# Kernel tuning notes

Measured on AMD Instinct MI355X. Metric: run time of the kernel, lower is better.

## Reference

```python
import jax, jax.numpy as jnp
import numpy as np

B, T, D = 2, 4096, 1024
H, HD = 16, 64
KV = H * HD  # 1024


def setup_inputs() -> dict:
    key = jax.random.key(0)
    ks = jax.random.split(key, 6)
    sc = lambda k, shape, s: jax.random.normal(k, shape, jnp.float32) * s
    return {
        "x": sc(ks[0], (B, T, D), 1.0),
        "W_in": sc(ks[1], (D, 4 * KV), D ** -0.5),      # in_proj (in, out) layout
        "W_ba": sc(ks[2], (D, 2 * H), D ** -0.5),       # ba_proj
        "conv_w": sc(ks[3], (3 * KV, 1, 4), 0.5),       # depthwise conv, (O, I/groups=1, K)
        "dt_bias": jnp.ones((H,), jnp.float32),
        "A_log": jnp.log(jax.random.uniform(ks[4], (H,), jnp.float32, 1e-3, 16.0)),
        "norm_w": jnp.ones((HD,), jnp.float32),
        "W_o": sc(ks[5], (KV, D), KV ** -0.5),
    }


def _l2norm(t, eps=1e-6):
    return t * jax.lax.rsqrt(jnp.sum(t * t, axis=-1, keepdims=True) + eps)


def reference(x, W_in, W_ba, conv_w, dt_bias, A_log, norm_w, W_o):
    Bb, Tt, _ = x.shape
    qkvz = x @ W_in                                  # [B,T,4*KV]
    q, k, v, z = jnp.split(qkvz, 4, axis=-1)
    b, a = jnp.split(x @ W_ba, 2, axis=-1)           # [B,T,H] each

    # causal depthwise conv (kernel 4, left pad 3) + SiLU on concat(q,k,v)
    qkv = jnp.concatenate([q, k, v], axis=-1).transpose(0, 2, 1)  # [B,3KV,T]
    qkv = jax.lax.conv_general_dilated(
        qkv, conv_w, window_strides=(1,), padding=[(3, 0)],
        feature_group_count=3 * KV, dimension_numbers=("NCH", "OIH", "NCH"))
    qkv = jax.nn.silu(qkv).transpose(0, 2, 1)        # [B,T,3KV]
    q, k, v = jnp.split(qkv, 3, axis=-1)

    rs = lambda t: t.reshape(Bb, Tt, H, HD)
    q, k, v, z = rs(q), rs(k), rs(v), rs(z)

    beta = jax.nn.sigmoid(b)                         # [B,T,H]
    A = jnp.exp(jnp.maximum(A_log, -2.3))            # [H]
    g = -A * jax.nn.softplus(a + dt_bias)            # [B,T,H], log decay <= 0

    # fla use_qk_l2norm_in_kernel=True: l2-normalize q,k; q scaled by d^-0.5
    q = _l2norm(q) * (HD ** -0.5)
    k = _l2norm(k)

    # gated delta rule recurrence over time (state S: [B,H,dk,dv])
    tm = lambda t: jnp.swapaxes(t, 0, 1)             # time-major

    def step(S, inp):
        qt, kt, vt, gt, bt = inp
        S = S * jnp.exp(gt)[..., None, None]
        pred = jnp.einsum("bhk,bhkv->bhv", kt, S)
        S = S + jnp.einsum("bhk,bhv->bhkv", kt, (vt - pred) * bt[..., None])
        o = jnp.einsum("bhk,bhkv->bhv", qt, S)
        return S, o

    S0 = jnp.zeros((Bb, H, HD, HD), jnp.float32)
    _, y = jax.lax.scan(step, S0, (tm(q), tm(k), tm(v), tm(g), tm(beta)))
    y = jnp.swapaxes(y, 0, 1)                        # [B,T,H,HD]

    # RMSNormGated over head_dim, gated by silu(z)
    y = y * jax.lax.rsqrt(jnp.mean(y * y, axis=-1, keepdims=True) + 1e-6)
    y = (norm_w * y) * jax.nn.silu(z)

    return y.reshape(Bb, Tt, KV) @ W_o
```

## Files before the change

kernel.cpp:

```cpp
#include <hip/hip_runtime.h>

typedef unsigned short u16;
typedef unsigned int u32;
typedef __attribute__((ext_vector_type(8))) __bf16 bf16x8;
typedef __attribute__((ext_vector_type(8))) _Float16 f16x8;
typedef __attribute__((ext_vector_type(4))) _Float16 f16x4;
typedef __attribute__((ext_vector_type(4))) float f32x4;

#define DEV __device__ __forceinline__

DEV u16 f2bf(float f) {
  u32 u = __float_as_uint(f);
  u += 0x7FFFu + ((u >> 16) & 1u);
  return (u16)(u >> 16);
}
DEV float bf2f(u16 h) { return __uint_as_float(((u32)h) << 16); }
DEV void splitbf(float f, u16& hi, u16& lo) {
  u16 h = f2bf(f);
  hi = h;
  lo = f2bf(f - bf2f(h));
}
DEV void split4(float4 v, ushort4& hh, ushort4& ll) {
  splitbf(v.x, hh.x, ll.x);
  splitbf(v.y, hh.y, ll.y);
// ... 334 lines not shown
  __syncthreads();
#pragma unroll
  for (int i = 0; i < 4; ++i)
#pragma unroll
    for (int j = 0; j < 4; ++j)
#pragma unroll
      for (int r = 0; r < 4; ++r) {
        int t = i * 16 + rbase + r, s = j * 16 + lrow;
        Af[t * 64 + s] = (s < t) ? bs[t] * expf(gcs[t] - gcs[s]) * acc[i][j][r] : 0.f;
      }
  __syncthreads();
  float x[64];
#pragma unroll
  for (int t = 0; t < 64; ++t) {
    float sum = 0.f;
#pragma unroll
    for (int s4 = 0; s4 + 4 <= t; s4 += 4) {
      float4 a4 = *(const float4*)&Af[t * 64 + s4];
      sum += a4.x * x[s4] + a4.y * x[s4 + 1] + a4.z * x[s4 + 2] + a4.w * x[s4 + 3];
    }
#pragma unroll
    for (int s = (t & ~3); s < t; ++s) sum += Af[t * 64 + s] * x[s];
    x[t] = ((t == lane) ? 1.f : 0.f) - sum;
  }
#pragma unroll
  for (int t = 0; t < 64; ++t) {
    u16 hi, lo;
    splitbf(x[t], hi, lo);
    Tgh[(size_t)bhc * 4096 + SW(t, lane)] = hi;
    Tgl[(size_t)bhc * 4096 + SW(t, lane)] = lo;
  }
}

__global__ __launch_bounds__(256) void k_mn(const u16* __restrict__ khG, const u16* __restrict__ klG,
                                            const u16* __restrict__ vhG, const u16* __restrict__ vlG,
                                            const u16* __restrict__ Tgh, const u16* __restrict__ Tgl,
                                            const float* __restrict__ gcG, const float* __restrict__ betaG,
                                            u16* __restrict__ Mh, u16* __restrict__ Ml,
                                            u16* __restrict__ Nh, u16* __restrict__ Nl) {
  extern __shared__ __align__(16) char smem[];
  u16* base = (u16*)smem;
  u16* Tbh  = base + 0 * 4096;
  u16* Tbl  = base + 1 * 4096;
  u16* X1h  = base + 2 * 4096;
  u16* X1l  = base + 3 * 4096;
  u16* KdTh = base + 4 * 4096;
  u16* KdTl = base + 5 * 4096;
  u16* X2h  = base + 6 * 4096;
  u16* X2l  = base + 7 * 4096;
  float* gcs = (float*)(base + 8 * 4096);
  float* bs  = gcs + 64;

  const int bhc = blockIdx.x;
  const int c = bhc & 63, h = (bhc >> 6) & 15, bb = bhc >> 10;
  const int tid = threadIdx.x, w = tid >> 6, l = tid & 63;
  const int lrow = l & 15, lk8 = (l >> 4) * 8, rbase = (l >> 4) * 4;
  const int t0 = c * 64;
  const size_t rowbase = (size_t)bb * 4096;
  const size_t ktile = (size_t)bhc * 4096;

  if (tid < 64) {
    gcs[tid] = gcG[(size_t)bhc * 64 + tid];
    bs[tid] = betaG[(rowbase + t0 + tid) * 16 + h];
  }
#pragma unroll
  for (int i = 0; i < 2; ++i) {
    const int idx = tid + 256 * i;
    const int off = idx * 8;
    *(float4*)&Tbh[off] = *(const float4*)&Tgh[(size_t)bhc * 4096 + off];
    *(float4*)&Tbl[off] = *(const float4*)&Tgl[(size_t)bhc * 4096 + off];
  }
  __syncthreads();
  const float gc63 = gcs[63];
#pragma unroll
  for (int i = 0; i < 16; ++i) {
    const int flat = tid + 256 * i;
    const int s = flat >> 6, d = flat & 63;
    const int sws = SW(s, d);
    const float kf = bf2f(khG[ktile + sws]) + bf2f(klG[ktile + sws]);
    const float gv = gcs[s], bv = bs[s];
    u16 hh, ll;
    splitbf(bv * expf(gv) * kf, hh, ll);
    X1h[SW(d, s)] = hh; X1l[SW(d, s)] = ll;
    splitbf(expf(gc63 - gv) * kf, hh, ll);
    KdTh[SW(d, s)] = hh; KdTl[SW(d, s)] = ll;
    const float vv = bf2f(vhG[ktile + sws]) + bf2f(vlG[ktile + sws]);
    splitbf(bv * vv, hh, ll);
    X2h[SW(d, s)] = hh; X2l[SW(d, s)] = ll;
  }
  __syncthreads();

  f32x4 aW[4], aU[4];
#pragma unroll
  for (int j = 0; j < 4; ++j) { aW[j] = {0.f,0.f,0.f,0.f}; aU[j] = {0.f,0.f,0.f,0.f}; }
#pragma unroll
  for (int ks = 0; ks < 2; ++ks) {
    const int ao = SW(w * 16 + lrow, ks * 32 + lk8);
    bf16x8 aTh = *(const bf16x8*)&Tbh[ao];
    bf16x8 aTl = *(const bf16x8*)&Tbl[ao];
#pragma unroll
    for (int j = 0; j < 4; ++j) {
      const int bo = SW(j * 16 + lrow, ks * 32 + lk8);
      aW[j] = mm3(aTh, aTl, *(const bf16x8*)&X1h[bo], *(const bf16x8*)&X1l[bo], aW[j]);
      aU[j] = mm3(aTh, aTl, *(const bf16x8*)&X2h[bo], *(const bf16x8*)&X2l[bo], aU[j]);
    }
  }
  __syncthreads();
#pragma unroll
  for (int j = 0; j < 4; ++j)
#pragma unroll
    for (int r = 0; r < 4; ++r) {
      const int t = w * 16 + rbase + r, dcol = j * 16 + lrow;
      u16 hh, ll;
      splitbf(aW[j][r], hh, ll);
      X1h[SW(dcol, t)] = hh; X1l[SW(dcol, t)] = ll;
      splitbf(aU[j][r], hh, ll);
      X2h[SW(dcol, t)] = hh; X2l[SW(dcol, t)] = ll;
    }
  __syncthreads();

  f32x4 aM[4], aN[4];
#pragma unroll
  for (int j = 0; j < 4; ++j) { aM[j] = {0.f,0.f,0.f,0.f}; aN[j] = {0.f,0.f,0.f,0.f}; }
#pragma unroll
  for (int ks = 0; ks < 2; ++ks) {
    const int ao = SW(w * 16 + lrow, ks * 32 + lk8);
    bf16x8 aKh = *(const bf16x8*)&KdTh[ao];
    bf16x8 aKl = *(const bf16x8*)&KdTl[ao];
#pragma unroll
    for (int j = 0; j < 4; ++j) {
      const int bo = SW(j * 16 + lrow, ks * 32 + lk8);
      aM[j] = mm3(aKh, aKl, *(const bf16x8*)&X1h[bo], *(const bf16x8*)&X1l[bo], aM[j]);
      aN[j] = mm3(aKh, aKl, *(const bf16x8*)&X2h[bo], *(const bf16x8*)&X2l[bo], aN[j]);
    }
  }
  __syncthreads();
  const float decC = expf(gc63);
#pragma unroll
  for (int j = 0; j < 4; ++j)
#pragma unroll
    for (int r = 0; r < 4; ++r) {
      const int d = w * 16 + rbase + r, d2 = j * 16 + lrow;
      u16 hh, ll;
      splitbf(((d == d2) ? decC : 0.f) - aM[j][r], hh, ll);
      X1h[SW(d, d2)] = hh; X1l[SW(d, d2)] = ll;
      splitbf(aN[j][r], hh, ll);
      X2h[SW(d, d2)] = hh; X2l[SW(d, d2)] = ll;
    }
  __syncthreads();
#pragma unroll
  for (int i = 0; i < 2; ++i) {
    const int idx = tid + 256 * i;
    const int off = idx * 8;
    *(float4*)&Mh[(size_t)bhc * 4096 + off] = *(const float4*)&X1h[off];
    *(float4*)&Ml[(size_t)bhc * 4096 + off] = *(const float4*)&X1l[off];
    *(float4*)&Nh[(size_t)bhc * 4096 + off] = *(const float4*)&X2h[off];
    *(float4*)&Nl[(size_t)bhc * 4096 + off] = *(const float4*)&X2l[off];
  }
}

__global__ __launch_bounds__(256) void k_seg(const u16* __restrict__ Mh, const u16* __restrict__ Ml,
                                             const u16* __restrict__ Nh, const u16* __restrict__ Nl,
                                             u16* __restrict__ Msegh, u16* __restrict__ Msegl,
                                             u16* __restrict__ Nsegh, u16* __restrict__ Nsegl) {
  extern __shared__ __align__(16) char smem[];
  u16* base = (u16*)smem;
  u16* MaTh = base + 0 * 4096;
  u16* MaTl = base + 1 * 4096;
  u16* NaTh = base + 2 * 4096;
  u16* NaTl = base + 3 * 4096;
  u16* sMh  = base + 4 * 4096;
  u16* sMl  = base + 5 * 4096;
  u16* sNh  = base + 6 * 4096;
  u16* sNl  = base + 7 * 4096;

  const int blk = blockIdx.x;
  const size_t cbase = (size_t)(blk >> 3) * 64 + (blk & 7) * 8;
  const int tid = threadIdx.x, w = tid >> 6, l = tid & 63;
  const int lrow = l & 15, lk8 = (l >> 4) * 8, rbase = (l >> 4) * 4;

#pragma unroll
  for (int i = 0; i < 2; ++i) {
    const int off = (tid + 256 * i) * 8;
    *(float4*)&sMh[off] = *(const float4*)&Mh[cbase * 4096 + off];
    *(float4*)&sMl[off] = *(const float4*)&Ml[cbase * 4096 + off];
    *(float4*)&sNh[off] = *(const float4*)&Nh[cbase * 4096 + off];
    *(float4*)&sNl[off] = *(const float4*)&Nl[cbase * 4096 + off];
  }
  __syncthreads();
#pragma unroll
  for (int i = 0; i < 16; ++i) {
    const int flat = tid + 256 * i;
    const int a = flat >> 6, b = flat & 63;
    MaTh[SW(a, b)] = sMh[SW(b, a)];
    MaTl[SW(a, b)] = sMl[SW(b, a)];
    NaTh[SW(a, b)] = sNh[SW(b, a)];
    NaTl[SW(a, b)] = sNl[SW(b, a)];
  }
  __syncthreads();

  for (int j = 1; j < 8; ++j) {
#pragma unroll
    for (int i = 0; i < 2; ++i) {
      const int off = (tid + 256 * i) * 8;
      *(float4*)&sMh[off] = *(const float4*)&Mh[(cbase + j) * 4096 + off];
      *(float4*)&sMl[off] = *(const float4*)&Ml[(cbase + j) * 4096 + off];
      *(float4*)&sNh[off] = *(const float4*)&Nh[(cbase + j) * 4096 + off];
      *(float4*)&sNl[off] = *(const float4*)&Nl[(cbase + j) * 4096 + off];
    }
    __syncthreads();
    f32x4 aM2[4], aN2[4];
#pragma unroll
    for (int jj = 0; jj < 4; ++jj) { aM2[jj] = {0.f,0.f,0.f,0.f}; aN2[jj] = {0.f,0.f,0.f,0.f}; }
#pragma unroll
    for (int ks = 0; ks < 2; ++ks) {
      const int ao = SW(w * 16 + lrow, ks * 32 + lk8);
      bf16x8 aCh = *(const bf16x8*)&sMh[ao];
      bf16x8 aCl = *(const bf16x8*)&sMl[ao];
#pragma unroll
      for (int jj = 0; jj < 4; ++jj) {
        const int bo = SW(jj * 16 + lrow, ks * 32 + lk8);
        aM2[jj] = mm3(aCh, aCl, *(const bf16x8*)&MaTh[bo], *(const bf16x8*)&MaTl[bo], aM2[jj]);
        aN2[jj] = mm3(aCh, aCl, *(const bf16x8*)&NaTh[bo], *(const bf16x8*)&NaTl[bo], aN2[jj]);
      }
    }
    __syncthreads();
#pragma unroll
    for (int jj = 0; jj < 4; ++jj)
#pragma unroll
      for (int r = 0; r < 4; ++r) {
        const int t = w * 16 + rbase + r, col = jj * 16 + lrow;
        u16 hh, ll;
        splitbf(aM2[jj][r], hh, ll);
        MaTh[SW(col, t)] = hh; MaTl[SW(col, t)] = ll;
        const float nv = aN2[jj][r] + bf2f(sNh[SW(t, col)]) + bf2f(sNl[SW(t, col)]);
        splitbf(nv, hh, ll);
        NaTh[SW(col, t)] = hh; NaTl[SW(col, t)] = ll;
      }
    __syncthreads();
  }
#pragma unroll
  for (int i = 0; i < 16; ++i) {
    const int flat = tid + 256 * i;
    const int t = flat >> 6, s = flat & 63;
    Msegh[(size_t)blk * 4096 + SW(t, s)] = MaTh[SW(s, t)];
    Msegl[(size_t)blk * 4096 + SW(t, s)] = MaTl[SW(s, t)];
    Nsegh[(size_t)blk * 4096 + SW(t, s)] = NaTh[SW(s, t)];
    Nsegl[(size_t)blk * 4096 + SW(t, s)] = NaTl[SW(s, t)];
  }
}

__global__ __launch_bounds__(256) void k_bound(const u16* __restrict__ Msegh, const u16* __restrict__ Msegl,
                                               const u16* __restrict__ Nsegh, const u16* __restrict__ Nsegl,
                                               u16* __restrict__ Ssegh, u16* __restrict__ Ssegl) {
  __shared__ __align__(16) u16 STh[4096], STl[4096];
  __shared__ __align__(16) u16 sMh[4096], sMl[4096], sNh[4096], sNl[4096];
  const int bh = blockIdx.x;
  const int tid = threadIdx.x, w = tid >> 6, l = tid & 63;
  const int lrow = l & 15, lk8 = (l >> 4) * 8, rbase = (l >> 4) * 4;
  for (int i = tid; i < 4096; i += 256) { STh[i] = (u16)0; STl[i] = (u16)0; }
  __syncthreads();
  for (int j = 0; j < 8; ++j) {
    const size_t sb = (size_t)(bh * 8 + j) * 4096;
#pragma unroll
    for (int i = 0; i < 2; ++i) {
      const int off = (tid + 256 * i) * 8;
      *(float4*)&Ssegh[sb + off] = *(const float4*)&STh[off];
      *(float4*)&Ssegl[sb + off] = *(const float4*)&STl[off];
      *(float4*)&sMh[off] = *(const float4*)&Msegh[sb + off];
      *(float4*)&sMl[off] = *(const float4*)&Msegl[sb + off];
      *(float4*)&sNh[off] = *(const float4*)&Nsegh[sb + off];
      *(float4*)&sNl[off] = *(const float4*)&Nsegl[sb + off];
    }
    __syncthreads();
    f32x4 acc[4];
#pragma unroll
    for (int jj = 0; jj < 4; ++jj) acc[jj] = {0.f, 0.f, 0.f, 0.f};
#pragma unroll
    for (int ks = 0; ks < 2; ++ks) {
      const int ao = SW(w * 16 + lrow, ks * 32 + lk8);
      bf16x8 aSh = *(const bf16x8*)&STh[ao];
      bf16x8 aSl = *(const bf16x8*)&STl[ao];
#pragma unroll
      for (int jj = 0; jj < 4; ++jj) {
        const int bo = SW(jj * 16 + lrow, ks * 32 + lk8);
        acc[jj] = mm3(aSh, aSl, *(const bf16x8*)&sMh[bo], *(const bf16x8*)&sMl[bo], acc[jj]);
      }
    }
    __syncthreads();
#pragma unroll
    for (int jj = 0; jj < 4; ++jj)
#pragma unroll
      for (int r = 0; r < 4; ++r) {
        const int v = w * 16 + rbase + r, t = jj * 16 + lrow;
        const float sv = acc[jj][r] + bf2f(sNh[SW(t, v)]) + bf2f(sNl[SW(t, v)]);
        u16 hh, ll;
        splitbf(sv, hh, ll);
        STh[SW(v, t)] = hh; STl[SW(v, t)] = ll;
      }
    __syncthreads();
  }
}

__global__ __launch_bounds__(256, 1) void k_scan2(const u16* __restrict__ qhG, const u16* __restrict__ qlG,
                                               const u16* __restrict__ khG, const u16* __restrict__ klG,
                                               const u16* __restrict__ vhG, const u16* __restrict__ vlG,
                                               const u16* __restrict__ zb,
                                               const u16* __restrict__ Tgh, const u16* __restrict__ Tgl,
                                               const float* __restrict__ gcG,
                                               const float* __restrict__ betaG, const float* __restrict__ norm_w,
                                               const u16* __restrict__ Ssegh, const u16* __restrict__ Ssegl,
                                               u16* __restrict__ Yhi, u16* __restrict__ Ylo) {
  extern __shared__ __align__(16) char smem[];
  u16* base = (u16*)smem;
  u16* Kbh  = base + 0 * 4096;
  u16* Kbl  = base + 1 * 4096;
  u16* Qbh  = base + 2 * 4096;
  u16* Qbl  = base + 3 * 4096;
  u16* Vbh  = base + 4 * 4096;
  u16* Vbl  = base + 5 * 4096;
  u16* Zb   = base + 6 * 4096;
  u16* Tbh  = base + 7 * 4096;
  u16* Tbl  = base + 8 * 4096;
  u16* SbTh = base + 9 * 4096;
  u16* SbTl = base + 10 * 4096;
  u16* Mqh  = base + 11 * 4096;
  u16* Mql  = base + 12 * 4096;
  u16* KdTh = base + 13 * 4096;
  u16* KdTl = base + 14 * 4096;
  u16* RTh  = base + 15 * 4096;
  u16* RTl  = base + 16 * 4096;
  u16* UTh  = base + 17 * 4096;
  u16* UTl  = base + 18 * 4096;
  u16* Ybh  = RTh;
  u16* Ybl  = RTl;
  float* gcs = (float*)(base + 19 * 4096);
  float* bs  = gcs + 64;
  float* nws = gcs + 128;

  const int blk = blockIdx.x;
  const int bh = blk >> 3, seg = blk & 7;
  const int bb = bh >> 4, h = bh & 15;
  const int tid = threadIdx.x, w = tid >> 6, l = tid & 63;
  const int lrow = l & 15, lk8 = (l >> 4) * 8, rbase = (l >> 4) * 4;
  const size_t rowbase = (size_t)bb * 4096;
  const size_t bhTile = (size_t)bh * 64;

  {
    const int c = seg * 8, t0 = c * 64;
    const size_t gt = (bhTile + c) * 4096;
#pragma unroll
    for (int i = 0; i < 2; ++i) {
      const int o8 = (tid + 256 * i) * 8;
      GLDS16(qhG + gt + o8, &Qbh[o8]);
      GLDS16(qlG + gt + o8, &Qbl[o8]);
      GLDS16(khG + gt + o8, &Kbh[o8]);
      GLDS16(klG + gt + o8, &Kbl[o8]);
      GLDS16(vhG + gt + o8, &Vbh[o8]);
      GLDS16(vlG + gt + o8, &Vbl[o8]);
      GLDS16(Tgh + (size_t)(bh * 64 + c) * 4096 + o8, &Tbh[o8]);
      GLDS16(Tgl + (size_t)(bh * 64 + c) * 4096 + o8, &Tbl[o8]);
      GLDS16(Ssegh + (size_t)blk * 4096 + o8, &SbTh[o8]);
      GLDS16(Ssegl + (size_t)blk * 4096 + o8, &SbTl[o8]);
    }
#pragma unroll
    for (int i = 0; i < 2; ++i) {
      const int idx = tid + 256 * i;
      const int r = idx >> 3, c8 = (idx & 7) << 3;
      *(float4*)&Zb[SW(r, c8)] = *(const float4*)&zb[(rowbase + t0 + r) * 1024 + h * 64 + c8];
    }
    if (tid < 64) {
      nws[tid] = norm_w[tid];
      gcs[tid] = gcG[((size_t)bh * 64 + c) * 64 + tid];
      bs[tid] = betaG[(rowbase + t0 + tid) * 16 + h];
    }
  }
  __syncthreads();

  for (int cc = 0; cc < 8; ++cc) {
    const int c = seg * 8 + cc;
    const int t0 = c * 64;
    const bool pf = (cc < 7);
    const size_t gt1 = (bhTile + c + 1) * 4096;

    float4 pz[2];
    float pgc = 0.f, pbs = 0.f;
    if (pf) {
      const int t1 = t0 + 64;
#pragma unroll
      for (int i = 0; i < 2; ++i) {
        const int idx = tid + 256 * i;
        const int r = idx >> 3, c8 = (idx & 7) << 3;
        pz[i] = *(const float4*)&zb[(rowbase + t1 + r) * 1024 + h * 64 + c8];
      }
      if (tid < 64) {
        pgc = gcG[((size_t)bh * 64 + (c + 1)) * 64 + tid];
        pbs = betaG[(rowbase + t1 + tid) * 16 + h];
      }
    }

    {
      const float gc63 = gcs[63];
#pragma unroll
      for (int i = 0; i < 16; ++i) {
        const int flat = tid * 16 + i;
        const int d = flat >> 6, s = flat & 63;
        const float kv = bf2f(Kbh[SW(s, d)]) + bf2f(Kbl[SW(s, d)]);
        u16 hh, ll;
        splitbf(expf(gc63 - gcs[s]) * kv, hh, ll);
        KdTh[SW(d, s)] = hh;
        KdTl[SW(d, s)] = ll;
      }
    }
    f32x4 aqk[4], ap[4], aqs[4];
#pragma unroll
    for (int j = 0; j < 4; ++j) { aqk[j] = {0.f,0.f,0.f,0.f}; ap[j] = {0.f,0.f,0.f,0.f}; aqs[j] = {0.f,0.f,0.f,0.f}; }
#pragma unroll
    for (int ks = 0; ks < 2; ++ks) {
      const int ao = SW(w * 16 + lrow, ks * 32 + lk8);
      bf16x8 aKh = *(const bf16x8*)&Kbh[ao];
      bf16x8 aKl = *(const bf16x8*)&Kbl[ao];
      bf16x8 aQh = *(const bf16x8*)&Qbh[ao];
      bf16x8 aQl = *(const bf16x8*)&Qbl[ao];
#pragma unroll
      for (int j = 0; j < 4; ++j) {
        const int bo = SW(j * 16 + lrow, ks * 32 + lk8);
        bf16x8 bKh = *(const bf16x8*)&Kbh[bo];
        bf16x8 bKl = *(const bf16x8*)&Kbl[bo];
        bf16x8 bSh = *(const bf16x8*)&SbTh[bo];
        bf16x8 bSl = *(const bf16x8*)&SbTl[bo];
        aqk[j] = mm3(aQh, aQl, bKh, bKl, aqk[j]);
        ap[j]  = mm3(aKh, aKl, bSh, bSl, ap[j]);
        aqs[j] = mm3(aQh, aQl, bSh, bSl, aqs[j]);
      }
    }
#pragma unroll
    for (int j = 0; j < 4; ++j)
#pragma unroll
      for (int r = 0; r < 4; ++r) {
        const int t = w * 16 + rbase + r;
        const int s = j * 16 + lrow;
        u16 mh, ml;
        splitbf((s <= t) ? expf(gcs[t] - gcs[s]) * aqk[j][r] : 0.f, mh, ml);
        Mqh[SW(t, s)] = mh;
        Mql[SW(t, s)] = ml;
        const float vv = bf2f(Vbh[SW(t, s)]) + bf2f(Vbl[SW(t, s)]);
        const float rhs = bs[t] * (vv - expf(gcs[t]) * ap[j][r]);
        u16 rh, rl;
        splitbf(rhs, rh, rl);
        RTh[SW(s, t)] = rh;
        RTl[SW(s, t)] = rl;
      }
    __syncthreads();

    if (pf) {
#pragma unroll
      for (int i = 0; i < 2; ++i) {
        const int o8 = (tid + 256 * i) * 8;
        GLDS16(qhG + gt1 + o8, &Qbh[o8]);
        GLDS16(qlG + gt1 + o8, &Qbl[o8]);
        GLDS16(khG + gt1 + o8, &Kbh[o8]);
        GLDS16(klG + gt1 + o8, &Kbl[o8]);
        GLDS16(vhG + gt1 + o8, &Vbh[o8]);
        GLDS16(vlG + gt1 + o8, &Vbl[o8]);
      }
    }

    f32x4 au[4];
#pragma unroll
    for (int j = 0; j < 4; ++j) au[j] = {0.f, 0.f, 0.f, 0.f};
#pragma unroll
    for (int ks = 0; ks < 2; ++ks) {
      const int ao = SW(w * 16 + lrow, ks * 32 + lk8);
      bf16x8 aTh = *(const bf16x8*)&Tbh[ao];
      bf16x8 aTl = *(const bf16x8*)&Tbl[ao];
#pragma unroll
      for (int j = 0; j < 4; ++j) {
        const int bo = SW(j * 16 + lrow, ks * 32 + lk8);
        au[j] = mm3(aTh, aTl, *(const bf16x8*)&RTh[bo], *(const bf16x8*)&RTl[bo], au[j]);
      }
    }
#pragma unroll
    for (int j = 0; j < 4; ++j)
#pragma unroll
      for (int r = 0; r < 4; ++r) {
        u16 uh, ul;
        splitbf(au[j][r], uh, ul);
        const int o = SW(j * 16 + lrow, w * 16 + rbase + r);
        UTh[o] = uh;
        UTl[o] = ul;
      }
    __syncthreads();

    if (pf) {
#pragma unroll
      for (int i = 0; i < 2; ++i) {
        const int o8 = (tid + 256 * i) * 8;
        GLDS16(Tgh + (size_t)(bh * 64 + (c + 1)) * 4096 + o8, &Tbh[o8]);
        GLDS16(Tgl + (size_t)(bh * 64 + (c + 1)) * 4096 + o8, &Tbl[o8]);
      }
    }

    f32x4 amu[4], as_[4];
#pragma unroll
    for (int j = 0; j < 4; ++j) { amu[j] = {0.f,0.f,0.f,0.f}; as_[j] = {0.f,0.f,0.f,0.f}; }
#pragma unroll
    for (int ks = 0; ks < 2; ++ks) {
      const int ao = SW(w * 16 + lrow, ks * 32 + lk8);
      bf16x8 aMh = *(const bf16x8*)&Mqh[ao];
      bf16x8 aMl = *(const bf16x8*)&Mql[ao];
      bf16x8 aKdh = *(const bf16x8*)&KdTh[ao];
      bf16x8 aKdl = *(const bf16x8*)&KdTl[ao];
#pragma unroll
      for (int j = 0; j < 4; ++j) {
        const int bo = SW(j * 16 + lrow, ks * 32 + lk8);
        bf16x8 bUh = *(const bf16x8*)&UTh[bo];
        bf16x8 bUl = *(const bf16x8*)&UTl[bo];
        amu[j] = mm3(aMh, aMl, bUh, bUl, amu[j]);
        as_[j] = mm3(aKdh, aKdl, bUh, bUl, as_[j]);
      }
    }
#pragma unroll
    for (int r = 0; r < 4; ++r) {
      const int t = w * 16 + rbase + r;
      const float gt = expf(gcs[t]);
      float y[4];
      float ss = 0.f;
#pragma unroll
      for (int j = 0; j < 4; ++j) { y[j] = gt * aqs[j][r] + amu[j][r]; ss += y[j] * y[j]; }
      ss += __shfl_xor(ss, 1); ss += __shfl_xor(ss, 2); ss += __shfl_xor(ss, 4); ss += __shfl_xor(ss, 8);
      const float rstd = rsqrtf(ss * (1.f / 64.f) + 1e-6f);
#pragma unroll
      for (int j = 0; j < 4; ++j) {
        const int col = j * 16 + lrow;
        const float zz = bf2f(Zb[SW(t, col)]);
        const float yv = y[j] * rstd * nws[col] * (zz / (1.f + expf(-zz)));
        u16 yh, yl;
        splitbf(yv, yh, yl);
        Ybh[SW(t, col)] = yh;
        Ybl[SW(t, col)] = yl;
      }
    }
    {
      const float decC = expf(gcs[63]);
#pragma unroll
      for (int j = 0; j < 4; ++j)
#pragma unroll
        for (int r = 0; r < 4; ++r) {
          const int d = w * 16 + rbase + r, col = j * 16 + lrow;
          const int o = SW(col, d);
          const float s0 = bf2f(SbTh[o]) + bf2f(SbTl[o]);
          const float sv = decC * s0 + as_[j][r];
          u16 sh, sl;
          splitbf(sv, sh, sl);
          SbTh[o] = sh;
          SbTl[o] = sl;
        }
    }
    __syncthreads();

#pragma unroll
    for (int i = 0; i < 2; ++i) {
      const int idx = tid + 256 * i;
      const int r = idx >> 3, c8 = (idx & 7) << 3;
      const size_t grow = (rowbase + t0 + r) * 1024 + h * 64 + c8;
      *(float4*)&Yhi[grow] = *(const float4*)&Ybh[SW(r, c8)];
      *(float4*)&Ylo[grow] = *(const float4*)&Ybl[SW(r, c8)];
    }
    if (pf) {
#pragma unroll
      for (int i = 0; i < 2; ++i) {
        const int idx = tid + 256 * i;
        const int r = idx >> 3, c8 = (idx & 7) << 3;
        *(float4*)&Zb[SW(r, c8)] = pz[i];
      }
      if (tid < 64) {
        gcs[tid] = pgc;
        bs[tid] = pbs;
      }
    }
    __syncthreads();
  }
}

extern "C" void kernel_launch(void* const* d_in, const int* in_sizes, int n_in,
                              void* d_out, int out_size, void* d_ws, size_t ws_size,
                              hipStream_t stream) {
  (void)in_sizes; (void)n_in; (void)out_size; (void)ws_size;
  const float* x       = (const float*)d_in[0];
  const float* W_in    = (const float*)d_in[1];
  const float* W_ba    = (const float*)d_in[2];
  const float* conv_w  = (const float*)d_in[3];
  const float* dt_bias = (const float*)d_in[4];
  const float* A_log   = (const float*)d_in[5];
  const float* norm_w  = (const float*)d_in[6];
  const float* W_o     = (const float*)d_in[7];
  float* out = (float*)d_out;
  char* ws = (char*)d_ws;
  const size_t MB = 1048576;

  _Float16* xh = (_Float16*)(ws + 0);
  u16* MhB   = (u16*)(ws + 0);
  u16* YhiB  = (u16*)(ws + 0);
  u16* MlB   = (u16*)(ws + 16 * MB);
  u16* YloB  = (u16*)(ws + 16 * MB);
  _Float16* WinT = (_Float16*)(ws + 32 * MB);
  float* gB  = (float*)(ws + 32 * MB);
  float* bB  = (float*)(ws + 32 * MB + 524288);
  float* gcB = (float*)(ws + 33 * MB);
  u16* Ssegh = (u16*)(ws + 34 * MB);
  u16* Ssegl = (u16*)(ws + 36 * MB);
  u16* Msegh = (u16*)(ws + 38 * MB);
  u16* Msegl = (u16*)(ws + 40 * MB);
  u16* Nsegh = (u16*)(ws + 42 * MB);
  u16* Nsegl = (u16*)(ws + 44 * MB);
  u16* WoT   = (u16*)(ws + 48 * MB);
  u16* qkv3  = (u16*)(ws + 50 * MB);
  u16* NhB   = (u16*)(ws + 50 * MB);
  u16* NlB   = (u16*)(ws + 66 * MB);
  u16* zbB   = (u16*)(ws + 98 * MB);
  u16* qhG   = (u16*)(ws + 114 * MB);
  u16* qlG   = (u16*)(ws + 130 * MB);
  u16* khG   = (u16*)(ws + 146 * MB);
  u16* klG   = (u16*)(ws + 162 * MB);
  u16* vhG   = (u16*)(ws + 178 * MB);
  u16* vlG   = (u16*)(ws + 194 * MB);
  u16* TghB  = (u16*)(ws + 210 * MB);
  u16* TglB  = (u16*)(ws + 226 * MB);

  const int SCAN_LDS = 19 * 8192 + 3 * 256;
  const int MN_LDS   = 8 * 8192 + 512;
  const int SEG_LDS  = 8 * 8192;

  k_cast_h<<<8192, 256, 0, stream>>>(x, xh, 8388608);
  k_transpose_h<<<dim3(64, 16), 256, 0, stream>>>(W_in, WinT, 1024, 4096);
  k_transpose<<<dim3(16, 16), 256, 0, stream>>>(W_o, WoT, 1024, 1024);
  k_gemm_h<<<dim3(32, 64), 256, 0, stream>>>(xh, WinT, qkv3, zbB, 8192, 4096, 1024);
  k_ba<<<2048, 256, 0, stream>>>(x, W_ba, dt_bias, A_log, bB, gB);
  k_conv<<<8192, 256, 0, stream>>>(qkv3, conv_w, qhG, qlG, khG, klG, vhG, vlG);
  k_prep<<<2048, 64, 0, stream>>>(khG, klG, gB, bB, gcB, TghB, TglB);
  hipFuncSetAttribute((const void*)k_mn, hipFuncAttributeMaxDynamicSharedMemorySize, MN_LDS);
  k_mn<<<2048, 256, MN_LDS, stream>>>(khG, klG, vhG, vlG, TghB, TglB, gcB, bB, MhB, MlB, NhB, NlB);
  hipFuncSetAttribute((const void*)k_seg, hipFuncAttributeMaxDynamicSharedMemorySize, SEG_LDS);
  k_seg<<<256, 256, SEG_LDS, stream>>>(MhB, MlB, NhB, NlB, Msegh, Msegl, Nsegh, Nsegl);
  k_bound<<<32, 256, 0, stream>>>(Msegh, Msegl, Nsegh, Nsegl, Ssegh, Ssegl);
  hipFuncSetAttribute((const void*)k_scan2, hipFuncAttributeMaxDynamicSharedMemorySize, SCAN_LDS);
  k_scan2<<<256, 256, SCAN_LDS, stream>>>(qhG, qlG, khG, klG, vhG, vlG, zbB, TghB, TglB, gcB, bB, norm_w,
                                          Ssegh, Ssegl, YhiB, YloB);
  k_gemm2<<<dim3(8, 64), 256, 0, stream>>>(YhiB, YloB, WoT, out, 8192, 1024, 1024);
}
```

Baseline: 541.3 us.

## Double k_scan2 block to 512 threads and precompute per-chunk decay exponentials

The chunked scan kernel now runs 8 waves per block instead of 4. Each pair of waves shares a 16-row strip and splits the output columns in half. Because the RMS-norm sum of squares is now spread across two waves, it is combined through a small LDS buffer with an extra barrier. The per-timestep decay exponentials exp(gc63-gc) and exp(gc) are computed once per chunk into LDS instead of being recomputed in the inner loops. The goal is more latency hiding in a kernel that has only 256 blocks, at the cost of more synchronisation and smaller per-wave MFMA tiles.

```diff
diff --git a/kernel.cpp b/kernel.cpp
--- a/kernel.cpp
+++ b/kernel.cpp
@@ -660,7 +660,7 @@
   }
 }
 
-__global__ __launch_bounds__(256, 1) void k_scan2(const u16* __restrict__ qhG, const u16* __restrict__ qlG,
+__global__ __launch_bounds__(512, 2) void k_scan2(const u16* __restrict__ qhG, const u16* __restrict__ qlG,
                                                const u16* __restrict__ khG, const u16* __restrict__ klG,
                                                const u16* __restrict__ vhG, const u16* __restrict__ vlG,
                                                const u16* __restrict__ zb,
@@ -695,42 +695,43 @@
   float* gcs = (float*)(base + 19 * 4096);
   float* bs  = gcs + 64;
   float* nws = gcs + 128;
+  float* esF = gcs + 192;
+  float* etF = gcs + 256;
+  float* ssP = gcs + 320;
 
   const int blk = blockIdx.x;
   const int bh = blk >> 3, seg = blk & 7;
   const int bb = bh >> 4, h = bh & 15;
   const int tid = threadIdx.x, w = tid >> 6, l = tid & 63;
+  const int wrow = w >> 1, jh = w & 1;
   const int lrow = l & 15, lk8 = (l >> 4) * 8, rbase = (l >> 4) * 4;
   const size_t rowbase = (size_t)bb * 4096;
   const size_t bhTile = (size_t)bh * 64;
+  const int o8 = tid * 8;
+  const int zr = tid >> 3, zc8 = (tid & 7) << 3;
 
   {
     const int c = seg * 8, t0 = c * 64;
     const size_t gt = (bhTile + c) * 4096;
-#pragma unroll
-    for (int i = 0; i < 2; ++i) {
-      const int o8 = (tid + 256 * i) * 8;
-      GLDS16(qhG + gt + o8, &Qbh[o8]);
-      GLDS16(qlG + gt + o8, &Qbl[o8]);
-      GLDS16(khG + gt + o8, &Kbh[o8]);
-      GLDS16(klG + gt + o8, &Kbl[o8]);
-      GLDS16(vhG + gt + o8, &Vbh[o8]);
-      GLDS16(vlG + gt + o8, &Vbl[o8]);
-      GLDS16(Tgh + (size_t)(bh * 64 + c) * 4096 + o8, &Tbh[o8]);
-      GLDS16(Tgl + (size_t)(bh * 64 + c) * 4096 + o8, &Tbl[o8]);
-      GLDS16(Ssegh + (size_t)blk * 4096 + o8, &SbTh[o8]);
-      GLDS16(Ssegl + (size_t)blk * 4096 + o8, &SbTl[o8]);
-    }
-#pragma unroll
-    for (int i = 0; i < 2; ++i) {
-      const int idx = tid + 256 * i;
-      const int r = idx >> 3, c8 = (idx & 7) << 3;
-      *(float4*)&Zb[SW(r, c8)] = *(const float4*)&zb[(rowbase + t0 + r) * 1024 + h * 64 + c8];
-    }
+    GLDS16(qhG + gt + o8, &Qbh[o8]);
+    GLDS16(qlG + gt + o8, &Qbl[o8]);
+    GLDS16(khG + gt + o8, &Kbh[o8]);
+    GLDS16(klG + gt + o8, &Kbl[o8]);
+    GLDS16(vhG + gt + o8, &Vbh[o8]);
+    GLDS16(vlG + gt + o8, &Vbl[o8]);
+    GLDS16(Tgh + (size_t)(bh * 64 + c) * 4096 + o8, &Tbh[o8]);
+    GLDS16(Tgl + (size_t)(bh * 64 + c) * 4096 + o8, &Tbl[o8]);
+    GLDS16(Ssegh + (size_t)blk * 4096 + o8, &SbTh[o8]);
+    GLDS16(Ssegl + (size_t)blk * 4096 + o8, &SbTl[o8]);
+    *(float4*)&Zb[SW(zr, zc8)] = *(const float4*)&zb[(rowbase + t0 + zr) * 1024 + h * 64 + zc8];
     if (tid < 64) {
       nws[tid] = norm_w[tid];
-      gcs[tid] = gcG[((size_t)bh * 64 + c) * 64 + tid];
-      bs[tid] = betaG[(rowbase + t0 + tid) * 16 + h];
+      float g0 = gcG[((size_t)bh * 64 + c) * 64 + tid];
+      float b0 = betaG[(rowbase + t0 + tid) * 16 + h];
+      float g63 = __shfl(g0, 63);
+      gcs[tid] = g0; bs[tid] = b0;
+      esF[tid] = expf(g63 - g0);
+      etF[tid] = expf(g0);
     }
   }
   __syncthreads();
@@ -741,48 +742,41 @@
     const bool pf = (cc < 7);
     const size_t gt1 = (bhTile + c + 1) * 4096;
 
-    float4 pz[2];
+    float4 pz;
     float pgc = 0.f, pbs = 0.f;
     if (pf) {
       const int t1 = t0 + 64;
-#pragma unroll
-      for (int i = 0; i < 2; ++i) {
-        const int idx = tid + 256 * i;
-        const int r = idx >> 3, c8 = (idx & 7) << 3;
-        pz[i] = *(const float4*)&zb[(rowbase + t1 + r) * 1024 + h * 64 + c8];
-      }
+      pz = *(const float4*)&zb[(rowbase + t1 + zr) * 1024 + h * 64 + zc8];
       if (tid < 64) {
         pgc = gcG[((size_t)bh * 64 + (c + 1)) * 64 + tid];
         pbs = betaG[(rowbase + t1 + tid) * 16 + h];
       }
     }
 
-    {
-      const float gc63 = gcs[63];
-#pragma unroll
-      for (int i = 0; i < 16; ++i) {
-        const int flat = tid * 16 + i;
-        const int d = flat >> 6, s = flat & 63;
-        const float kv = bf2f(Kbh[SW(s, d)]) + bf2f(Kbl[SW(s, d)]);
-        u16 hh, ll;
-        splitbf(expf(gc63 - gcs[s]) * kv, hh, ll);
-        KdTh[SW(d, s)] = hh;
-        KdTl[SW(d, s)] = ll;
-      }
-    }
-    f32x4 aqk[4], ap[4], aqs[4];
-#pragma unroll
-    for (int j = 0; j < 4; ++j) { aqk[j] = {0.f,0.f,0.f,0.f}; ap[j] = {0.f,0.f,0.f,0.f}; aqs[j] = {0.f,0.f,0.f,0.f}; }
+#pragma unroll
+    for (int i = 0; i < 8; ++i) {
+      const int flat = tid * 8 + i;
+      const int d = flat >> 6, s = flat & 63;
+      const float kv = bf2f(Kbh[SW(s, d)]) + bf2f(Kbl[SW(s, d)]);
+      u16 hh, ll;
+      splitbf(esF[s] * kv, hh, ll);
+      KdTh[SW(d, s)] = hh;
+      KdTl[SW(d, s)] = ll;
+    }
+    f32x4 aqk[2], ap[2], aqs[2];
+#pragma unroll
+    for (int j = 0; j < 2; ++j) { aqk[j] = {0.f,0.f,0.f,0.f}; ap[j] = {0.f,0.f,0.f,0.f}; aqs[j] = {0.f,0.f,0.f,0.f}; }
 #pragma unroll
     for (int ks = 0; ks < 2; ++ks) {
-      const int ao = SW(w * 16 + lrow, ks * 32 + lk8);
+      const int ao = SW(wrow * 16 + lrow, ks * 32 + lk8);
       bf16x8 aKh = *(const bf16x8*)&Kbh[ao];
       bf16x8 aKl = *(const bf16x8*)&Kbl[ao];
       bf16x8 aQh = *(const bf16x8*)&Qbh[ao];
       bf16x8 aQl = *(const bf16x8*)&Qbl[ao];
 #pragma unroll
-      for (int j = 0; j < 4; ++j) {
-        const int bo = SW(j * 16 + lrow, ks * 32 + lk8);
+      for (int j = 0; j < 2; ++j) {
+        const int jj = jh * 2 + j;
+        const int bo = SW(jj * 16 + lrow, ks * 32 + lk8);
         bf16x8 bKh = *(const bf16x8*)&Kbh[bo];
         bf16x8 bKl = *(const bf16x8*)&Kbl[bo];
         bf16x8 bSh = *(const bf16x8*)&SbTh[bo];
@@ -793,17 +787,17 @@
       }
     }
 #pragma unroll
-    for (int j = 0; j < 4; ++j)
+    for (int j = 0; j < 2; ++j)
 #pragma unroll
       for (int r = 0; r < 4; ++r) {
-        const int t = w * 16 + rbase + r;
-        const int s = j * 16 + lrow;
+        const int t = wrow * 16 + rbase + r;
+        const int s = (jh * 2 + j) * 16 + lrow;
         u16 mh, ml;
         splitbf((s <= t) ? expf(gcs[t] - gcs[s]) * aqk[j][r] : 0.f, mh, ml);
         Mqh[SW(t, s)] = mh;
         Mql[SW(t, s)] = ml;
         const float vv = bf2f(Vbh[SW(t, s)]) + bf2f(Vbl[SW(t, s)]);
-        const float rhs = bs[t] * (vv - expf(gcs[t]) * ap[j][r]);
+        const float rhs = bs[t] * (vv - etF[t] * ap[j][r]);
         u16 rh, rl;
         splitbf(rhs, rh, rl);
         RTh[SW(s, t)] = rh;
@@ -812,87 +806,88 @@
     __syncthreads();
 
     if (pf) {
-#pragma unroll
-      for (int i = 0; i < 2; ++i) {
-        const int o8 = (tid + 256 * i) * 8;
-        GLDS16(qhG + gt1 + o8, &Qbh[o8]);
-        GLDS16(qlG + gt1 + o8, &Qbl[o8]);
-        GLDS16(khG + gt1 + o8, &Kbh[o8]);
-        GLDS16(klG + gt1 + o8, &Kbl[o8]);
-        GLDS16(vhG + gt1 + o8, &Vbh[o8]);
-        GLDS16(vlG + gt1 + o8, &Vbl[o8]);
-      }
-    }
-
-    f32x4 au[4];
-#pragma unroll
-    for (int j = 0; j < 4; ++j) au[j] = {0.f, 0.f, 0.f, 0.f};
+      GLDS16(qhG + gt1 + o8, &Qbh[o8]);
+      GLDS16(qlG + gt1 + o8, &Qbl[o8]);
+      GLDS16(khG + gt1 + o8, &Kbh[o8]);
+      GLDS16(klG + gt1 + o8, &Kbl[o8]);
+      GLDS16(vhG + gt1 + o8, &Vbh[o8]);
+      GLDS16(vlG + gt1 + o8, &Vbl[o8]);
+    }
+
+    f32x4 au[2];
+#pragma unroll
+    for (int j = 0; j < 2; ++j) au[j] = {0.f, 0.f, 0.f, 0.f};
 #pragma unroll
     for (int ks = 0; ks < 2; ++ks) {
-      const int ao = SW(w * 16 + lrow, ks * 32 + lk8);
+      const int ao = SW(wrow * 16 + lrow, ks * 32 + lk8);
       bf16x8 aTh = *(const bf16x8*)&Tbh[ao];
       bf16x8 aTl = *(const bf16x8*)&Tbl[ao];
 #pragma unroll
-      for (int j = 0; j < 4; ++j) {
-        const int bo = SW(j * 16 + lrow, ks * 32 + lk8);
+      for (int j = 0; j < 2; ++j) {
+        const int bo = SW((jh * 2 + j) * 16 + lrow, ks * 32 + lk8);
         au[j] = mm3(aTh, aTl, *(const bf16x8*)&RTh[bo], *(const bf16x8*)&RTl[bo], au[j]);
       }
     }
 #pragma unroll
-    for (int j = 0; j < 4; ++j)
+    for (int j = 0; j < 2; ++j)
 #pragma unroll
       for (int r = 0; r < 4; ++r) {
         u16 uh, ul;
         splitbf(au[j][r], uh, ul);
-        const int o = SW(j * 16 + lrow, w * 16 + rbase + r);
+        const int o = SW((jh * 2 + j) * 16 + lrow, wrow * 16 + rbase + r);
         UTh[o] = uh;
         UTl[o] = ul;
       }
     __syncthreads();
 
     if (pf) {
-#pragma unroll
-      for (int i = 0; i < 2; ++i) {
-        const int o8 = (tid + 256 * i) * 8;
-        GLDS16(Tgh + (size_t)(bh * 64 + (c + 1)) * 4096 + o8, &Tbh[o8]);
-        GLDS16(Tgl + (size_t)(bh * 64 + (c + 1)) * 4096 + o8, &Tbl[o8]);
-      }
-    }
-
-    f32x4 amu[4], as_[4];
-#pragma unroll
-    for (int j = 0; j < 4; ++j) { amu[j] = {0.f,0.f,0.f,0.f}; as_[j] = {0.f,0.f,0.f,0.f}; }
+      GLDS16(Tgh + (size_t)(bh * 64 + (c + 1)) * 4096 + o8, &Tbh[o8]);
+      GLDS16(Tgl + (size_t)(bh * 64 + (c + 1)) * 4096 + o8, &Tbl[o8]);
+    }
+
+    f32x4 amu[2], as_[2];
+#pragma unroll
+    for (int j = 0; j < 2; ++j) { amu[j] = {0.f,0.f,0.f,0.f}; as_[j] = {0.f,0.f,0.f,0.f}; }
 #pragma unroll
     for (int ks = 0; ks < 2; ++ks) {
-      const int ao = SW(w * 16 + lrow, ks * 32 + lk8);
+      const int ao = SW(wrow * 16 + lrow, ks * 32 + lk8);
       bf16x8 aMh = *(const bf16x8*)&Mqh[ao];
       bf16x8 aMl = *(const bf16x8*)&Mql[ao];
       bf16x8 aKdh = *(const bf16x8*)&KdTh[ao];
       bf16x8 aKdl = *(const bf16x8*)&KdTl[ao];
 #pragma unroll
-      for (int j = 0; j < 4; ++j) {
-        const int bo = SW(j * 16 + lrow, ks * 32 + lk8);
+      for (int j = 0; j < 2; ++j) {
+        const int bo = SW((jh * 2 + j) * 16 + lrow, ks * 32 + lk8);
         bf16x8 bUh = *(const bf16x8*)&UTh[bo];
         bf16x8 bUl = *(const bf16x8*)&UTl[bo];
         amu[j] = mm3(aMh, aMl, bUh, bUl, amu[j]);
         as_[j] = mm3(aKdh, aKdl, bUh, bUl, as_[j]);
       }
     }
+    float yv_[4][2];
 #pragma unroll
     for (int r = 0; r < 4; ++r) {
-      const int t = w * 16 + rbase + r;
-      const float gt = expf(gcs[t]);
-      float y[4];
+      const int t = wrow * 16 + rbase + r;
+      const float gt = etF[t];
       float ss = 0.f;
 #pragma unroll
-      for (int j = 0; j < 4; ++j) { y[j] = gt * aqs[j][r] + amu[j][r]; ss += y[j] * y[j]; }
+      for (int j = 0; j < 2; ++j) {
+        yv_[r][j] = gt * aqs[j][r] + amu[j][r];
+        ss += yv_[r][j] * yv_[r][j];
+      }
       ss += __shfl_xor(ss, 1); ss += __shfl_xor(ss, 2); ss += __shfl_xor(ss, 4); ss += __shfl_xor(ss, 8);
-      const float rstd = rsqrtf(ss * (1.f / 64.f) + 1e-6f);
-#pragma unroll
-      for (int j = 0; j < 4; ++j) {
-        const int col = j * 16 + lrow;
+      if (lrow == 0) ssP[jh * 64 + t] = ss;
+    }
+    __syncthreads();
+#pragma unroll
+    for (int r = 0; r < 4; ++r) {
+      const int t = wrow * 16 + rbase + r;
+      const float rstd = rsqrtf((ssP[t] + ssP[64 + t]) * (1.f / 64.f) + 1e-6f);
+#pragma unroll
+      for (int j = 0; j < 2; ++j) {
+        const int col = (jh * 2 + j) * 16 + lrow;
         const float zz = bf2f(Zb[SW(t, col)]);
-        const float yv = y[j] * rstd * nws[col] * (zz / (1.f + expf(-zz)));
+        const float yv = yv_[r][j] * rstd * nws[col] * (zz / (1.f + expf(-zz)));
         u16 yh, yl;
         splitbf(yv, yh, yl);
         Ybh[SW(t, col)] = yh;
@@ -900,12 +895,12 @@
       }
     }
     {
-      const float decC = expf(gcs[63]);
-#pragma unroll
-      for (int j = 0; j < 4; ++j)
+      const float decC = etF[63];
+#pragma unroll
+      for (int j = 0; j < 2; ++j)
 #pragma unroll
         for (int r = 0; r < 4; ++r) {
-          const int d = w * 16 + rbase + r, col = j * 16 + lrow;
+          const int d = wrow * 16 + rbase + r, col = (jh * 2 + j) * 16 + lrow;
           const int o = SW(col, d);
           const float s0 = bf2f(SbTh[o]) + bf2f(SbTl[o]);
           const float sv = decC * s0 + as_[j][r];
@@ -917,24 +912,18 @@
     }
     __syncthreads();
 
-#pragma unroll
-    for (int i = 0; i < 2; ++i) {
-      const int idx = tid + 256 * i;
-      const int r = idx >> 3, c8 = (idx & 7) << 3;
-      const size_t grow = (rowbase + t0 + r) * 1024 + h * 64 + c8;
-      *(float4*)&Yhi[grow] = *(const float4*)&Ybh[SW(r, c8)];
-      *(float4*)&Ylo[grow] = *(const float4*)&Ybl[SW(r, c8)];
+    {
+      const size_t grow = (rowbase + t0 + zr) * 1024 + h * 64 + zc8;
+      *(float4*)&Yhi[grow] = *(const float4*)&Ybh[SW(zr, zc8)];
+      *(float4*)&Ylo[grow] = *(const float4*)&Ybl[SW(zr, zc8)];
     }
     if (pf) {
-#pragma unroll
-      for (int i = 0; i < 2; ++i) {
-        const int idx = tid + 256 * i;
-        const int r = idx >> 3, c8 = (idx & 7) << 3;
-        *(float4*)&Zb[SW(r, c8)] = pz[i];
-      }
+      *(float4*)&Zb[SW(zr, zc8)] = pz;
       if (tid < 64) {
-        gcs[tid] = pgc;
-        bs[tid] = pbs;
+        float g63 = __shfl(pgc, 63);
+        gcs[tid] = pgc; bs[tid] = pbs;
+        esF[tid] = expf(g63 - pgc);
+        etF[tid] = expf(pgc);
       }
     }
     __syncthreads();
@@ -986,7 +975,7 @@
   u16* TghB  = (u16*)(ws + 210 * MB);
   u16* TglB  = (u16*)(ws + 226 * MB);
 
-  const int SCAN_LDS = 19 * 8192 + 3 * 256;
+  const int SCAN_LDS = 19 * 8192 + 448 * 4;
   const int MN_LDS   = 8 * 8192 + 512;
   const int SEG_LDS  = 8 * 8192;
 
@@ -1003,7 +992,7 @@
   k_seg<<<256, 256, SEG_LDS, stream>>>(MhB, MlB, NhB, NlB, Msegh, Msegl, Nsegh, Nsegl);
   k_bound<<<32, 256, 0, stream>>>(Msegh, Msegl, Nsegh, Nsegl, Ssegh, Ssegl);
   hipFuncSetAttribute((const void*)k_scan2, hipFuncAttributeMaxDynamicSharedMemorySize, SCAN_LDS);
-  k_scan2<<<256, 256, SCAN_LDS, stream>>>(qhG, qlG, khG, klG, vhG, vlG, zbB, TghB, TglB, gcB, bB, norm_w,
+  k_scan2<<<256, 512, SCAN_LDS, stream>>>(qhG, qlG, khG, klG, vhG, vlG, zbB, TghB, TglB, gcB, bB, norm_w,
                                           Ssegh, Ssegl, YhiB, YloB);
   k_gemm2<<<dim3(8, 64), 256, 0, stream>>>(YhiB, YloB, WoT, out, 8192, 1024, 1024);
 }
```

Measured after the change: 528.7 us. 2.3% less time.
